# Performance work log

Measured on AMD Instinct MI355X. Metric: run time of the kernel, lower is better.

The kernel has to match this reference:

```python
import jax, jax.numpy as jnp
import numpy as np

# Santacoder-style MQA transformer, prefill path (equal-length ragged batch)
B, S, D, H, L, FF, V, P = 2, 1024, 2048, 16, 2, 8192, 32000, 8192
HD = D // H               # head_size = 128
EPS = 1e-5
SCALE = HD ** -0.5


def _ln(x, g, b):
    mu = jnp.mean(x, axis=-1, keepdims=True)
    var = jnp.mean(jnp.square(x - mu), axis=-1, keepdims=True)
    return (x - mu) * jax.lax.rsqrt(var + EPS) * g + b


def setup_inputs() -> dict:
    key = jax.random.key(0)
    ks = jax.random.split(key, 8)
    f = lambda k, shape: jax.random.normal(k, shape, dtype=jnp.float32) * 0.02
    return {
        'input_ids': jax.random.randint(ks[0], (B * S,), 0, V),
        'position_ids': jnp.tile(jnp.arange(S), B),
        'wte': f(ks[1], (V, D)),
        'wpe': f(ks[2], (P, D)),
        'c_attn_w': f(ks[3], (L, D, D + 2 * HD)),
        'c_attn_b': jnp.zeros((L, D + 2 * HD), jnp.float32),
        'c_proj_w': f(ks[4], (L, D, D)),
        'c_proj_b': jnp.zeros((L, D), jnp.float32),
        'ln1_w': jnp.ones((L, D), jnp.float32),
        'ln1_b': jnp.zeros((L, D), jnp.float32),
        'ln2_w': jnp.ones((L, D), jnp.float32),
        'ln2_b': jnp.zeros((L, D), jnp.float32),
        'fc_w': f(ks[5], (L, D, FF)),
        'fc_b': jnp.zeros((L, FF), jnp.float32),
        'mp_w': f(ks[6], (L, FF, D)),
        'mp_b': jnp.zeros((L, D), jnp.float32),
        'lnf_w': jnp.ones((D,), jnp.float32),
        'lnf_b': jnp.zeros((D,), jnp.float32),
    }


def _forward(input_ids, position_ids, wte, wpe, c_attn_w, c_attn_b, c_proj_w,
             c_proj_b, ln1_w, ln1_b, ln2_w, ln2_b, fc_w, fc_b, mp_w, mp_b,
             lnf_w, lnf_b):
    T = input_ids.shape[0]                       # total ragged tokens = B*S
    h = wte[input_ids] + wpe[position_ids]       # [T, D]
    causal = jnp.tril(jnp.ones((S, S), dtype=bool))  # per-sequence causal mask
    residual = None
    for l in range(L):
        # FastLayerNorm: fused residual-add + layernorm
        res = h if residual is None else h + residual
        x = _ln(res, ln1_w[l], ln1_b[l])
        # MQA: one query group of H heads, a single shared KV head
        qkv = x @ c_attn_w[l] + c_attn_b[l]       # [T, D + 2*HD]
        q = qkv[:, :D].reshape(B, S, H, HD)
        k = qkv[:, D:D + HD].reshape(B, S, HD)    # single KV head (broadcast over H)
        v = qkv[:, D + HD:].reshape(B, S, HD)
        scores = jnp.einsum('bqhd,bkd->bhqk', q, k) * SCALE
        scores = jnp.where(causal, scores, jnp.finfo(scores.dtype).min)
        probs = jax.nn.softmax(scores, axis=-1)
        ctx = jnp.einsum('bhqk,bkd->bqhd', probs, v).reshape(T, D)
        attn_out = ctx @ c_proj_w[l] + c_proj_b[l]
        res2 = attn_out + res
        x2 = _ln(res2, ln2_w[l], ln2_b[l])
        # gelu_pytorch_tanh -> tanh-approximate gelu
        mlp = jax.nn.gelu(x2 @ fc_w[l] + fc_b[l], approximate=True) @ mp_w[l] + mp_b[l]
        h, residual = mlp, res2
    return _ln(h + residual, lnf_w, lnf_b)        # [T, D]


def reference(input_ids, position_ids, wte, wpe, c_attn_w, c_attn_b, c_proj_w,
              c_proj_b, ln1_w, ln1_b, ln2_w, ln2_b, fc_w, fc_b, mp_w, mp_b,
              lnf_w, lnf_b):
    return _forward(input_ids, position_ids, wte, wpe, c_attn_w, c_attn_b,
                    c_proj_w, c_proj_b, ln1_w, ln1_b, ln2_w, ln2_b, fc_w,
                    fc_b, mp_w, mp_b, lnf_w, lnf_b)
```

## Files before the change

kernel.cpp:

```cpp
#include <hip/hip_runtime.h>
#include <math.h>


typedef __bf16 bf16x8 __attribute__((ext_vector_type(8)));
typedef __bf16 bf16x4v __attribute__((ext_vector_type(4)));
typedef float floatx4 __attribute__((ext_vector_type(4)));

typedef const __attribute__((address_space(1))) void* gas_ptr;
typedef __attribute__((address_space(3))) void* las_ptr;

__device__ __forceinline__ void glds16(const __bf16* g, __bf16* l) {
  __builtin_amdgcn_global_load_lds((gas_ptr)g, (las_ptr)l, 16, 0, 0);
}

__device__ __forceinline__ float gelu_tanh(float x) {
  float u = 0.7978845608028654f * (x + 0.044715f * x * x * x);
  return 0.5f * x * (1.f + tanhf(u));
}

__global__ __launch_bounds__(256)
void embed_kernel(const int* __restrict__ ids, const int* __restrict__ pos,
                  const float* __restrict__ wte, const float* __restrict__ wpe,
                  float* __restrict__ out)
{
  const int t = blockIdx.x;
  const int id = ids[t], pp = pos[t];
  const float4* a = (const float4*)(wte + (size_t)id * 2048);
  const float4* b = (const float4*)(wpe + (size_t)pp * 2048);
  float4* o = (float4*)(out + (size_t)t * 2048);
#pragma unroll
  for (int j = 0; j < 2; j++) {
    int i = threadIdx.x + j * 256;
    float4 x = a[i], y = b[i];
    x.x += y.x; x.y += y.y; x.z += y.z; x.w += y.w;
    o[i] = x;
  }
}

__global__ __launch_bounds__(256)
void wcvt_kernel(const float* __restrict__ in, __bf16* __restrict__ out,
                 const int K, const int N)
{
  __shared__ __bf16 tile[32][36];
  const int n0 = blockIdx.x * 32, k0 = blockIdx.y * 32;
  const int t = threadIdx.x;
  const int r = t >> 3, c = (t & 7) * 4;
  const float4 v = *(const float4*)&in[(size_t)(k0 + r) * N + n0 + c];
  tile[r][c + 0] = (__bf16)v.x;
  tile[r][c + 1] = (__bf16)v.y;
  tile[r][c + 2] = (__bf16)v.z;
  tile[r][c + 3] = (__bf16)v.w;
  __syncthreads();
  bf16x4v w;
  w.x = tile[c + 0][r]; w.y = tile[c + 1][r];
  w.z = tile[c + 2][r]; w.w = tile[c + 3][r];
  *(bf16x4v*)&out[(size_t)(n0 + r) * K + k0 + c] = w;
}

__global__ __launch_bounds__(256)
void vtr_kernel(const __bf16* __restrict__ qkvb, __bf16* __restrict__ vT)
{
  __shared__ __bf16 tile[32][36];
  const int d0 = blockIdx.x * 32, s0 = blockIdx.y * 32, b = blockIdx.z;
  const int t = threadIdx.x;
  const int r = t >> 3, c = (t & 7) * 4;
  bf16x4v v = *(const bf16x4v*)&qkvb[(size_t)(b * 1024 + s0 + r) * 2304 + 2176 + d0 + c];
  tile[r][c + 0] = v.x; tile[r][c + 1] = v.y;
  tile[r][c + 2] = v.z; tile[r][c + 3] = v.w;
  __syncthreads();
  bf16x4v w;
  w.x = tile[c + 0][r]; w.y = tile[c + 1][r];
  w.z = tile[c + 2][r]; w.w = tile[c + 3][r];
  *(bf16x4v*)&vT[(size_t)b * 131072 + (size_t)(d0 + r) * 1024 + s0 + c] = w;
}

__global__ __launch_bounds__(256)
void ln_red_kernel(const float* __restrict__ p0, const float* __restrict__ p1,
                   const float* __restrict__ p2, const float* __restrict__ p3,
                   const float* __restrict__ cbias, const float* __restrict__ resid,
                   float* __restrict__ res_out, __bf16* __restrict__ out_b,
                   float* __restrict__ out_f,
                   const float* __restrict__ gw, const float* __restrict__ gb)
{
  const int row = blockIdx.x;
  const int tid = threadIdx.x;
  const size_t base = (size_t)row * 2048;
  float4 v[2];
  float s = 0.f, sq = 0.f;
#pragma unroll
  for (int j = 0; j < 2; j++) {
    const int idx = tid + j * 256;
    float4 a = ((const float4*)(p0 + base))[idx];
    if (p1) { float4 t = ((const float4*)(p1 + base))[idx];
      a.x += t.x; a.y += t.y; a.z += t.z; a.w += t.w; }
    if (p2) { float4 t = ((const float4*)(p2 + base))[idx];
      a.x += t.x; a.y += t.y; a.z += t.z; a.w += t.w; }
    if (p3) { float4 t = ((const float4*)(p3 + base))[idx];
      a.x += t.x; a.y += t.y; a.z += t.z; a.w += t.w; }
    if (cbias) { float4 t = ((const float4*)cbias)[idx];
      a.x += t.x; a.y += t.y; a.z += t.z; a.w += t.w; }
    if (resid) { float4 t = ((const float4*)(resid + base))[idx];
      a.x += t.x; a.y += t.y; a.z += t.z; a.w += t.w; }
    if (res_out) ((float4*)(res_out + base))[idx] = a;
    v[j] = a;
    s  += a.x + a.y + a.z + a.w;
    sq += a.x * a.x + a.y * a.y + a.z * a.z + a.w * a.w;
  }
  __shared__ float rs[4], rq[4];
  __shared__ float sh_stats[2];
#pragma unroll
  for (int off = 32; off > 0; off >>= 1) {
    s  += __shfl_down(s, off);
    sq += __shfl_down(sq, off);
  }
  const int lane = tid & 63, wave = tid >> 6;
  if (lane == 0) { rs[wave] = s; rq[wave] = sq; }
  __syncthreads();
  if (tid == 0) {
    float S = rs[0] + rs[1] + rs[2] + rs[3];
    float Q = rq[0] + rq[1] + rq[2] + rq[3];
    float mean = S * (1.f / 2048.f);
    float var  = Q * (1.f / 2048.f) - mean * mean;
    sh_stats[0] = mean;
    sh_stats[1] = rsqrtf(var + 1e-5f);
  }
  __syncthreads();
  const float mean = sh_stats[0], rstd = sh_stats[1];
#pragma unroll
  for (int j = 0; j < 2; j++) {
    const int idx = tid + j * 256;
    float4 a = v[j];
    float4 g4 = ((const float4*)gw)[idx];
    float4 b4 = ((const float4*)gb)[idx];
    float y0 = (a.x - mean) * rstd * g4.x + b4.x;
    float y1 = (a.y - mean) * rstd * g4.y + b4.y;
    float y2 = (a.z - mean) * rstd * g4.z + b4.z;
    float y3 = (a.w - mean) * rstd * g4.w + b4.w;
    if (out_b) {
      bf16x4v w;
      w.x = (__bf16)y0; w.y = (__bf16)y1; w.z = (__bf16)y2; w.w = (__bf16)y3;
      *(bf16x4v*)&out_b[base + (size_t)idx * 4] = w;
    }
    if (out_f) {
      float4 w; w.x = y0; w.y = y1; w.z = y2; w.w = y3;
      ((float4*)(out_f + base))[idx] = w;
    }
  }
}

__global__ __launch_bounds__(256)
void bias_red_bf16_kernel(const float* __restrict__ p0, const float* __restrict__ p1,
                          const float* __restrict__ bias, __bf16* __restrict__ out)
{
  const size_t i = ((size_t)blockIdx.x * 256 + threadIdx.x) * 4;
  const int col = (int)(i % 2304);
  float4 a = *(const float4*)(p0 + i);
  const float4 b = *(const float4*)(p1 + i);
  const float4 c = *(const float4*)(bias + col);
  bf16x4v w;
  w.x = (__bf16)(a.x + b.x + c.x);
  w.y = (__bf16)(a.y + b.y + c.y);
  w.z = (__bf16)(a.z + b.z + c.z);
  w.w = (__bf16)(a.w + b.w + c.w);
  *(bf16x4v*)(out + i) = w;
}

template<int MODE>
__global__ __launch_bounds__(256)
void gemm_bt_kernel(const __bf16* __restrict__ A, const __bf16* __restrict__ Bt,
                    const float* __restrict__ bias, void* __restrict__ Cout,
                    const int M, const int N, const int K, const int Kper)
{
  __shared__ __bf16 As[128 * 32];
  __shared__ __bf16 Bs[128 * 32];
  const int tid  = threadIdx.x;
  const int lane = tid & 63;
  const int wave = tid >> 6;
  const int col  = lane & 15;
  const int quad = lane >> 4;
  const int m0 = blockIdx.y * 128;
  const int n0 = blockIdx.x * 128;
  const int wm = (wave & 1) * 64;
  const int wn = (wave >> 1) * 64;
  const int s  = blockIdx.z;
  floatx4 acc[4][4] = {};

  const int srow = tid >> 2;
  const int scol = (tid & 3) * 8;
  const __bf16* Ag = A  + (size_t)s * Kper + (size_t)(m0 + srow) * K + scol;
  const __bf16* Bg = Bt + (size_t)s * Kper + (size_t)(n0 + srow) * K + scol;
  const size_t rowskip = (size_t)64 * K;

  for (int k0 = 0; k0 < Kper; k0 += 32) {
    glds16(Ag + k0,           As + tid * 8);
    glds16(Ag + k0 + rowskip, As + 2048 + tid * 8);
    glds16(Bg + k0,           Bs + tid * 8);
    glds16(Bg + k0 + rowskip, Bs + 2048 + tid * 8);
    __syncthreads();
    bf16x8 af[4], bf[4];
#pragma unroll
    for (int mi = 0; mi < 4; mi++)
      af[mi] = *(const bf16x8*)&As[(wm + mi * 16 + col) * 32 + quad * 8];
#pragma unroll
    for (int ni = 0; ni < 4; ni++)
      bf[ni] = *(const bf16x8*)&Bs[(wn + ni * 16 + col) * 32 + quad * 8];
#pragma unroll
    for (int mi = 0; mi < 4; mi++)
#pragma unroll
      for (int ni = 0; ni < 4; ni++)
        acc[mi][ni] = __builtin_amdgcn_mfma_f32_16x16x32_bf16(af[mi], bf[ni], acc[mi][ni], 0, 0, 0);
    __syncthreads();
  }

  float* Cp = (MODE == 3) ? ((float*)Cout + (size_t)s * M * N) : (float*)Cout;
#pragma unroll
  for (int ni = 0; ni < 4; ni++) {
    const int cc = n0 + wn + ni * 16 + col;
    const float bv = (MODE == 3) ? 0.f : bias[cc];
#pragma unroll
    for (int mi = 0; mi < 4; mi++) {
#pragma unroll
      for (int r = 0; r < 4; r++) {
        const int rr = m0 + wm + mi * 16 + quad * 4 + r;
        float v = acc[mi][ni][r] + bv;
        if constexpr (MODE == 2) v = gelu_tanh(v);
        if constexpr (MODE == 0 || MODE == 3)
          Cp[(size_t)rr * N + cc] = v;
        else
          ((__bf16*)Cout)[(size_t)rr * N + cc] = (__bf16)v;
      }
    }
  }
}

__global__ __launch_bounds__(256)
void flash_kernel(const __bf16* __restrict__ qkv, const __bf16* __restrict__ vT,
                  __bf16* __restrict__ ctx)
{
  const int qt = blockIdx.x, h = blockIdx.y, b = blockIdx.z;
  const int tid  = threadIdx.x;
  const int lane = tid & 63, wave = tid >> 6;
  const int col  = lane & 15, quad = lane >> 4;
  __shared__ __bf16 Qs[64 * 128];
  __shared__ __bf16 Ks[64 * 128];
  __shared__ __bf16 Vs[128 * 64];
  __shared__ __bf16 Ps[4][16 * 64];

#pragma unroll
  for (int p = 0; p < 4; p++) {
    int c = tid + p * 256;
    glds16(qkv + (size_t)(b * 1024 + qt * 64 + (c >> 4)) * 2304 + h * 128 + (c & 15) * 8,
           Qs + c * 8);
  }

  float m_i[4], l_i[4];
  floatx4 o[8] = {};
#pragma unroll
  for (int r = 0; r < 4; r++) { m_i[r] = -1e30f; l_i[r] = 0.f; }

  for (int kt = 0; kt <= qt; kt++) {
    __syncthreads();
#pragma unroll
    for (int p = 0; p < 4; p++) {
      int c = tid + p * 256;
      glds16(qkv + (size_t)(b * 1024 + kt * 64 + (c >> 4)) * 2304 + 2048 + (c & 15) * 8,
             Ks + c * 8);
    }
#pragma unroll
    for (int p = 0; p < 4; p++) {
      int c = tid + p * 256;
      glds16(vT + (size_t)b * 131072 + (size_t)(c >> 3) * 1024 + kt * 64 + (c & 7) * 8,
             Vs + c * 8);
    }
    __syncthreads();

    floatx4 sc[4] = {};
#pragma unroll
    for (int kk = 0; kk < 4; kk++) {
      bf16x8 qa = *(const bf16x8*)&Qs[(wave * 16 + col) * 128 + kk * 32 + quad * 8];
#pragma unroll
      for (int ni = 0; ni < 4; ni++) {
        bf16x8 kb = *(const bf16x8*)&Ks[(ni * 16 + col) * 128 + kk * 32 + quad * 8];
        sc[ni] = __builtin_amdgcn_mfma_f32_16x16x32_bf16(qa, kb, sc[ni], 0, 0, 0);
      }
    }

    const bool diag = (kt == qt);
#pragma unroll
    for (int r = 0; r < 4; r++) {
      const int rowL = wave * 16 + quad * 4 + r;
      float mx = -1e30f;
#pragma unroll
      for (int ni = 0; ni < 4; ni++) {
        float s = sc[ni][r] * 0.08838834764831845f;
        if (diag && (ni * 16 + col) > rowL) s = -1e30f;
        sc[ni][r] = s;
        mx = fmaxf(mx, s);
      }
#pragma unroll
      for (int off = 1; off < 16; off <<= 1) mx = fmaxf(mx, __shfl_xor(mx, off));
      const float mnew = fmaxf(m_i[r], mx);
      const float alpha = __expf(m_i[r] - mnew);
      l_i[r] *= alpha;
      float rsum = 0.f;
#pragma unroll
      for (int ni = 0; ni < 4; ni++) {
        float p = __expf(sc[ni][r] - mnew);
        sc[ni][r] = p;
        rsum += p;
      }
#pragma unroll
      for (int off = 1; off < 16; off <<= 1) rsum += __shfl_xor(rsum, off);
      l_i[r] += rsum;
      m_i[r] = mnew;
#pragma unroll
      for (int nd = 0; nd < 8; nd++) o[nd][r] *= alpha;
    }

    __bf16* Pw = &Ps[wave][0];
#pragma unroll
    for (int r = 0; r < 4; r++)
#pragma unroll
      for (int ni = 0; ni < 4; ni++)
        Pw[(quad * 4 + r) * 64 + ni * 16 + col] = (__bf16)sc[ni][r];

#pragma unroll
    for (int kk = 0; kk < 2; kk++) {
      bf16x8 pa = *(const bf16x8*)&Pw[col * 64 + kk * 32 + quad * 8];
#pragma unroll
      for (int nd = 0; nd < 8; nd++) {
        bf16x8 vb = *(const bf16x8*)&Vs[(nd * 16 + col) * 64 + kk * 32 + quad * 8];
        o[nd] = __builtin_amdgcn_mfma_f32_16x16x32_bf16(pa, vb, o[nd], 0, 0, 0);
      }
    }
  }

#pragma unroll
  for (int r = 0; r < 4; r++) {
    const float inv = 1.f / l_i[r];
    const int row = qt * 64 + wave * 16 + quad * 4 + r;
    const size_t base = (size_t)(b * 1024 + row) * 2048 + h * 128;
#pragma unroll
    for (int nd = 0; nd < 8; nd++)
      ctx[base + nd * 16 + col] = (__bf16)(o[nd][r] * inv);
  }
}

extern "C" void kernel_launch(void* const* d_in, const int* in_sizes, int n_in,
                              void* d_out, int out_size, void* d_ws, size_t ws_size,
                              hipStream_t stream)
{
  (void)in_sizes; (void)n_in; (void)out_size; (void)ws_size;
  const int*   ids = (const int*)d_in[0];
  const int*   pos = (const int*)d_in[1];
  const float* wte = (const float*)d_in[2];
  const float* wpe = (const float*)d_in[3];
  const float* caw = (const float*)d_in[4];
  const float* cab = (const float*)d_in[5];
  const float* cpw = (const float*)d_in[6];
  const float* cpb = (const float*)d_in[7];
  const float* l1w = (const float*)d_in[8];
  const float* l1b = (const float*)d_in[9];
  const float* l2w = (const float*)d_in[10];
  const float* l2b = (const float*)d_in[11];
  const float* fcw = (const float*)d_in[12];
  const float* fcb = (const float*)d_in[13];
  const float* mpw = (const float*)d_in[14];
  const float* mpb = (const float*)d_in[15];
  const float* lfw = (const float*)d_in[16];
  const float* lfb = (const float*)d_in[17];
  float* out = (float*)d_out;

  char* ws = (char*)d_ws;
  float*  resA  = (float*)(ws + 0);
  float*  resB  = (float*)(ws + 16777216);
  __bf16* xb    = (__bf16*)(ws + 33554432);
  __bf16* qkvb  = (__bf16*)(ws + 41943040);
  __bf16* ctxb  = (__bf16*)(ws + 51380224);
  __bf16* vtb   = (__bf16*)(ws + 59768832);
  __bf16* wqkvT = (__bf16*)(ws + 60293120);
  __bf16* wprjT = (__bf16*)(ws + 69730304);
  __bf16* wfcT  = (__bf16*)(ws + 78118912);
  __bf16* wmpT  = (__bf16*)(ws + 111673344);
  char*   arena = ws + 145227776;
  float*  pq    = (float*)arena;
  float*  pp    = (float*)arena;
  __bf16* mlp1b = (__bf16*)arena;
  float*  pm    = (float*)(ws + 182976512);

  const size_t MN  = (size_t)2048 * 2048;
  const size_t MNq = (size_t)2048 * 2304;

  embed_kernel<<<2048, 256, 0, stream>>>(ids, pos, wte, wpe, resA);

  for (int l = 0; l < 2; l++) {
    if (l == 0)
      ln_red_kernel<<<2048, 256, 0, stream>>>(
          resA, nullptr, nullptr, nullptr, nullptr, nullptr,
          nullptr, xb, nullptr, l1w, l1b);
    else
      ln_red_kernel<<<2048, 256, 0, stream>>>(
          pm, pm + MN, pm + 2 * MN, pm + 3 * MN, mpb, resB,
          resA, xb, nullptr, l1w + 2048, l1b + 2048);

    wcvt_kernel<<<dim3(72, 64), 256, 0, stream>>>(caw + (size_t)l * 2048 * 2304,
                                                  wqkvT, 2048, 2304);
    gemm_bt_kernel<3><<<dim3(18, 16, 2), 256, 0, stream>>>(
        xb, wqkvT, nullptr, pq, 2048, 2304, 2048, 1024);
    bias_red_bf16_kernel<<<4608, 256, 0, stream>>>(pq, pq + MNq, cab + l * 2304, qkvb);

    vtr_kernel<<<dim3(4, 32, 2), 256, 0, stream>>>(qkvb, vtb);
    flash_kernel<<<dim3(16, 16, 2), 256, 0, stream>>>(qkvb, vtb, ctxb);

    wcvt_kernel<<<dim3(64, 64), 256, 0, stream>>>(cpw + (size_t)l * 2048 * 2048,
                                                  wprjT, 2048, 2048);
    gemm_bt_kernel<3><<<dim3(16, 16, 2), 256, 0, stream>>>(
        ctxb, wprjT, nullptr, pp, 2048, 2048, 2048, 1024);
    ln_red_kernel<<<2048, 256, 0, stream>>>(
        pp, pp + MN, nullptr, nullptr, cpb + l * 2048, resA,
        resB, xb, nullptr, l2w + l * 2048, l2b + l * 2048);

    wcvt_kernel<<<dim3(256, 64), 256, 0, stream>>>(fcw + (size_t)l * 2048 * 8192,
                                                   wfcT, 2048, 8192);
    gemm_bt_kernel<2><<<dim3(64, 16, 1), 256, 0, stream>>>(
        xb, wfcT, fcb + l * 8192, mlp1b, 2048, 8192, 2048, 2048);

    wcvt_kernel<<<dim3(64, 256), 256, 0, stream>>>(mpw + (size_t)l * 8192 * 2048,
                                                   wmpT, 8192, 2048);
    gemm_bt_kernel<3><<<dim3(16, 16, 4), 256, 0, stream>>>(
        mlp1b, wmpT, nullptr, pm, 2048, 2048, 8192, 2048);
  }

  ln_red_kernel<<<2048, 256, 0, stream>>>(
      pm, pm + MN, pm + 2 * MN, pm + 3 * MN, mpb + 2048, resB,
      nullptr, nullptr, out, lfw, lfb);
}
```

Before: 1.448 ms.

## Add 256x256-tile double-buffered GEMM kernel for projection and MLP matmuls

Introduces a 512-thread GEMM with 256x256 output tiles, a swizzled LDS layout, direct global-to-LDS loads, two-slot prefetch, and MFMA priority hints. It replaces the old GEMM for the attention output projection (now split-K 4, writing into the pm partial buffers) and both MLP matmuls. The larger tiles raise arithmetic intensity per LDS byte, but the grids shrink to 256 blocks, which may underfill the device. The extra split-K partials for c_proj also add reduction traffic in the layernorm kernel.

```diff
diff --git a/kernel.cpp b/kernel.cpp
--- a/kernel.cpp
+++ b/kernel.cpp
@@ -226,6 +226,133 @@
         if constexpr (MODE == 2) v = gelu_tanh(v);
         if constexpr (MODE == 0 || MODE == 3)
           Cp[(size_t)rr * N + cc] = v;
+        else
+          ((__bf16*)Cout)[(size_t)rr * N + cc] = (__bf16)v;
+      }
+    }
+  }
+}
+
+template<int MODE>
+__global__ __launch_bounds__(512, 2)
+void gemm256_kernel(const __bf16* __restrict__ A, const __bf16* __restrict__ Bt,
+                    const float* __restrict__ bias, void* __restrict__ Cout,
+                    const int M, const int N, const int K, const int Kper)
+{
+  __shared__ alignas(16) __bf16 sm[65536];
+  const int tid  = threadIdx.x;
+  const int lane = tid & 63;
+  const int wave = tid >> 6;
+  const int col  = lane & 15;
+  const int quad = lane >> 4;
+  const int wm = (wave >> 2) * 128;
+  const int wn = (wave & 3) * 64;
+  const int m0 = blockIdx.y * 256;
+  const int n0 = blockIdx.x * 256;
+  const int ksplit = blockIdx.z;
+
+  const __bf16* Ag = A  + (size_t)m0 * K + (size_t)ksplit * Kper;
+  const __bf16* Bg = Bt + (size_t)n0 * K + (size_t)ksplit * Kper;
+
+  const int sr = tid >> 3;
+  const int sc = (((tid & 7) ^ (sr & 7)) * 8);
+  const int ld = tid * 8;
+
+  const int roff0 = (((0 | quad) ^ (col & 7)) * 8);
+  const int roff1 = (((4 | quad) ^ (col & 7)) * 8);
+
+  const int NT = Kper / 64;
+
+  auto stage = [&](int t, int slot) {
+    __bf16* dA = sm + slot * 32768;
+    __bf16* dB = dA + 16384;
+    const __bf16* gA = Ag + t * 64;
+    const __bf16* gB = Bg + t * 64;
+#pragma unroll
+    for (int i = 0; i < 4; i++)
+      glds16(gA + (size_t)(i * 64 + sr) * K + sc, dA + i * 4096 + ld);
+#pragma unroll
+    for (int i = 0; i < 4; i++)
+      glds16(gB + (size_t)(i * 64 + sr) * K + sc, dB + i * 4096 + ld);
+  };
+
+  floatx4 acc[8][4] = {};
+
+  stage(0, 0);
+  stage(1, 1);
+  asm volatile("s_waitcnt vmcnt(8)" ::: "memory");
+  __builtin_amdgcn_s_barrier();
+  __builtin_amdgcn_sched_barrier(0);
+
+  for (int t = 0; t < NT; t++) {
+    const int slot = t & 1;
+    const __bf16* As = sm + slot * 32768;
+    const __bf16* Bs = As + 16384;
+    bf16x8 af[8][2], bf[4][2];
+#pragma unroll
+    for (int ni = 0; ni < 4; ni++) {
+      bf[ni][0] = *(const bf16x8*)&Bs[(wn + ni * 16 + col) * 64 + roff0];
+      bf[ni][1] = *(const bf16x8*)&Bs[(wn + ni * 16 + col) * 64 + roff1];
+    }
+#pragma unroll
+    for (int mi = 0; mi < 4; mi++) {
+      af[mi][0] = *(const bf16x8*)&As[(wm + mi * 16 + col) * 64 + roff0];
+      af[mi][1] = *(const bf16x8*)&As[(wm + mi * 16 + col) * 64 + roff1];
+    }
+    __builtin_amdgcn_s_setprio(1);
+#pragma unroll
+    for (int mi = 0; mi < 4; mi++)
+#pragma unroll
+      for (int ni = 0; ni < 4; ni++)
+#pragma unroll
+        for (int ks = 0; ks < 2; ks++)
+          acc[mi][ni] = __builtin_amdgcn_mfma_f32_16x16x32_bf16(
+              af[mi][ks], bf[ni][ks], acc[mi][ni], 0, 0, 0);
+    __builtin_amdgcn_s_setprio(0);
+#pragma unroll
+    for (int mi = 4; mi < 8; mi++) {
+      af[mi][0] = *(const bf16x8*)&As[(wm + mi * 16 + col) * 64 + roff0];
+      af[mi][1] = *(const bf16x8*)&As[(wm + mi * 16 + col) * 64 + roff1];
+    }
+    asm volatile("s_waitcnt lgkmcnt(0)" ::: "memory");
+    __builtin_amdgcn_s_barrier();
+    __builtin_amdgcn_sched_barrier(0);
+    if (t + 2 < NT) stage(t + 2, slot);
+    __builtin_amdgcn_sched_barrier(0);
+    __builtin_amdgcn_s_setprio(1);
+#pragma unroll
+    for (int mi = 4; mi < 8; mi++)
+#pragma unroll
+      for (int ni = 0; ni < 4; ni++)
+#pragma unroll
+        for (int ks = 0; ks < 2; ks++)
+          acc[mi][ni] = __builtin_amdgcn_mfma_f32_16x16x32_bf16(
+              af[mi][ks], bf[ni][ks], acc[mi][ni], 0, 0, 0);
+    __builtin_amdgcn_s_setprio(0);
+    if (t + 1 < NT) {
+      if (t + 2 < NT)
+        asm volatile("s_waitcnt vmcnt(8)" ::: "memory");
+      else
+        asm volatile("s_waitcnt vmcnt(0)" ::: "memory");
+      __builtin_amdgcn_s_barrier();
+      __builtin_amdgcn_sched_barrier(0);
+    }
+  }
+
+  float* Cpf = (MODE == 3) ? ((float*)Cout + (size_t)ksplit * M * N) : (float*)Cout;
+#pragma unroll
+  for (int ni = 0; ni < 4; ni++) {
+    const int cc = n0 + wn + ni * 16 + col;
+    const float bv = (MODE == 3) ? 0.f : bias[cc];
+#pragma unroll
+    for (int mi = 0; mi < 8; mi++) {
+#pragma unroll
+      for (int r = 0; r < 4; r++) {
+        const int rr = m0 + wm + mi * 16 + quad * 4 + r;
+        float v = acc[mi][ni][r] + bv;
+        if constexpr (MODE == 2) v = gelu_tanh(v);
+        if constexpr (MODE == 3)
+          Cpf[(size_t)rr * N + cc] = v;
         else
           ((__bf16*)Cout)[(size_t)rr * N + cc] = (__bf16)v;
       }
@@ -384,7 +511,6 @@
   __bf16* wmpT  = (__bf16*)(ws + 111673344);
   char*   arena = ws + 145227776;
   float*  pq    = (float*)arena;
-  float*  pp    = (float*)arena;
   __bf16* mlp1b = (__bf16*)arena;
   float*  pm    = (float*)(ws + 182976512);
 
@@ -414,20 +540,20 @@
 
     wcvt_kernel<<<dim3(64, 64), 256, 0, stream>>>(cpw + (size_t)l * 2048 * 2048,
                                                   wprjT, 2048, 2048);
-    gemm_bt_kernel<3><<<dim3(16, 16, 2), 256, 0, stream>>>(
-        ctxb, wprjT, nullptr, pp, 2048, 2048, 2048, 1024);
+    gemm256_kernel<3><<<dim3(8, 8, 4), 512, 0, stream>>>(
+        ctxb, wprjT, nullptr, pm, 2048, 2048, 2048, 512);
     ln_red_kernel<<<2048, 256, 0, stream>>>(
-        pp, pp + MN, nullptr, nullptr, cpb + l * 2048, resA,
+        pm, pm + MN, pm + 2 * MN, pm + 3 * MN, cpb + l * 2048, resA,
         resB, xb, nullptr, l2w + l * 2048, l2b + l * 2048);
 
     wcvt_kernel<<<dim3(256, 64), 256, 0, stream>>>(fcw + (size_t)l * 2048 * 8192,
                                                    wfcT, 2048, 8192);
-    gemm_bt_kernel<2><<<dim3(64, 16, 1), 256, 0, stream>>>(
+    gemm256_kernel<2><<<dim3(32, 8, 1), 512, 0, stream>>>(
         xb, wfcT, fcb + l * 8192, mlp1b, 2048, 8192, 2048, 2048);
 
     wcvt_kernel<<<dim3(64, 256), 256, 0, stream>>>(mpw + (size_t)l * 8192 * 2048,
                                                    wmpT, 8192, 2048);
-    gemm_bt_kernel<3><<<dim3(16, 16, 4), 256, 0, stream>>>(
+    gemm256_kernel<3><<<dim3(8, 8, 4), 512, 0, stream>>>(
         mlp1b, wmpT, nullptr, pm, 2048, 2048, 8192, 2048);
   }
 
```

After: 1.249 ms. 13.8% less time.
